# Kernel optimization log

Hardware: AMD Instinct MI355X
Metric: run time of the kernel (lower is better)

## Reference

```python
import jax, jax.numpy as jnp
import numpy as np

B, NUM, FEAT, H = 32, 512, 1024, 8
HLEN = FEAT // H  # 128


def setup_inputs() -> dict:
    key = jax.random.key(0)
    ks = jax.random.split(key, 9)
    x1 = jax.random.normal(ks[0], (B, NUM, FEAT), dtype=jnp.float32)
    x2 = jax.random.normal(ks[1], (B, NUM, FEAT), dtype=jnp.float32)
    adj = jax.random.uniform(ks[2], (B, NUM, NUM), dtype=jnp.float32)
    bias = jax.random.normal(ks[3], (B, NUM, NUM), dtype=jnp.float32)
    mask = jax.random.bernoulli(ks[4], 0.1, (B, 1, NUM, NUM))  # bool
    # per-head projection weights: FCNet([feat, hdim], '', 0.1) == Linear(feat, hdim)
    Wq = jax.random.normal(ks[5], (H, FEAT, HLEN), dtype=jnp.float32) * (1.0 / np.sqrt(FEAT))
    bq = jnp.zeros((H, HLEN), dtype=jnp.float32)
    # output FCNet([feat, feat], 'ReLU', 0.1) == Linear(feat, feat) + ReLU
    Wl = jax.random.normal(ks[6], (FEAT, FEAT), dtype=jnp.float32) * (1.0 / np.sqrt(FEAT))
    bl = jnp.zeros((FEAT,), dtype=jnp.float32)
    return {"x1": x1, "x2": x2, "adj": adj, "bias": bias, "mask": mask,
            "Wq": Wq, "bq": bq, "Wl": Wl, "bl": bl}


def reference(x1, x2, adj, bias, mask, Wq, bq, Wl, bl):
    # adj and bias are unused in the original forward.
    Bsz, num, feat = x1.shape
    h_len = feat // H
    # Q: concat of per-head Linear(feat, h_len) projections -> [B, num, feat],
    # then split into H heads of h_len: [B, H, num, h_len]
    Q = jnp.einsum('bnf,hfd->bhnd', x1, Wq) + bq[None, :, None, :]
    # K = V = x1 reshaped into heads
    K = x1.reshape(Bsz, num, H, h_len).transpose(0, 2, 1, 3)  # [B,H,num,h_len]
    V = K
    # gate: average pool x2 over its sequence dim -> [B, feat] -> [B,H,1,h_len]
    gate = jnp.mean(x2, axis=1).reshape(Bsz, 1, H, h_len).transpose(0, 2, 1, 3)
    scale = 1.0 / np.sqrt(float(h_len))
    aff = jnp.einsum('bhnd,bhmd->bhnm', Q * gate, K * gate) * scale
    L = jnp.where(mask, jnp.float32(-1e9), aff)
    att = jax.nn.softmax(L, axis=3)  # [B,H,num,num]
    V_ = jnp.einsum('bhnm,bhmd->bhnd', att, V)
    V_ = V_.transpose(0, 2, 1, 3).reshape(Bsz, num, feat)
    xout = jax.nn.relu(V_ @ Wl + bl) + x1
    return (xout, att)
```

## Files before the change

kernel.cpp:

```cpp
#include <hip/hip_runtime.h>
#include <hip/hip_bf16.h>

typedef __attribute__((ext_vector_type(8))) short s8v;
typedef __attribute__((ext_vector_type(4))) float f4v;
typedef __hip_bfloat16 bf16;

__device__ __forceinline__ unsigned short f2b(float f) {
  bf16 h = __float2bfloat16(f);
  return *reinterpret_cast<unsigned short*>(&h);
}

__global__ __launch_bounds__(256) void gate_kernel(const float* __restrict__ x2,
                                                   float* __restrict__ g2s) {
  __shared__ float red[256];
  const int b = blockIdx.x >> 4, fc = blockIdx.x & 15;
  const int fi = threadIdx.x & 63, ng = threadIdx.x >> 6;
  const int f = fc * 64 + fi;
  const float* p = x2 + (size_t)b * 524288 + f;
  float s = 0.f;
  for (int n = ng * 128; n < ng * 128 + 128; ++n) s += p[(size_t)n * 1024];
  red[threadIdx.x] = s;
  __syncthreads();
  if (threadIdx.x < 64) {
    float tot = red[fi] + red[fi + 64] + red[fi + 128] + red[fi + 192];
    float mean = tot * (1.0f / 512.0f);
    g2s[b * 1024 + f] = mean * mean * 0.08838834764831845f;
  }
}

__global__ __launch_bounds__(256) void cvt_f32_bf16(const float* __restrict__ in,
                                                    bf16* __restrict__ out, int n4) {
  int i = blockIdx.x * 256 + threadIdx.x;
  if (i >= n4) return;
  f4v v = reinterpret_cast<const f4v*>(in)[i];
  ushort4 o;
  o.x = f2b(v.x); o.y = f2b(v.y); o.z = f2b(v.z); o.w = f2b(v.w);
  reinterpret_cast<ushort4*>(out)[i] = o;
}

__global__ __launch_bounds__(256) void transpose_f32_bf16(
    const float* __restrict__ in, bf16* __restrict__ out,
    int in_rstride, int out_rstride, int hi_shift,
    long hi_mul, long lo_mul, long out_mul) {
  __shared__ float tile[32][33];
  const int z = blockIdx.z;
  const long in_off = (long)(z >> hi_shift) * hi_mul + (long)(z & ((1 << hi_shift) - 1)) * lo_mul;
  const int r0 = blockIdx.x * 32, c0 = blockIdx.y * 32;
  const int i = threadIdx.x >> 5, j = threadIdx.x & 31;
  const float* ip = in + in_off + (long)r0 * in_rstride + c0;
#pragma unroll
  for (int s = 0; s < 4; ++s) tile[i + s * 8][j] = ip[(long)(i + s * 8) * in_rstride + j];
  __syncthreads();
  bf16* op = out + (long)z * out_mul + (long)c0 * out_rstride + r0;
#pragma unroll
  for (int s = 0; s < 4; ++s) op[(long)(i + s * 8) * out_rstride + j] = __float2bfloat16(tile[j][i + s * 8]);
}

template <int EPI>
__global__ __launch_bounds__(256) void gemm_nt(
    const void* __restrict__ Ap, const bf16* __restrict__ BTp, void* __restrict__ Op,
    const float* __restrict__ e1, const float* __restrict__ e2,
    int K, int lda, int ldb) {
  constexpr bool AF32 = (EPI == 1);
  __shared__ alignas(16) bf16 As[128 * 40];
  __shared__ alignas(16) bf16 Bs[128 * 40];
  const int t = threadIdx.x;
  const int lane = t & 63;
  const int w = t >> 6;
  const int wr = w >> 1, wc = w & 1;
  const int lr = lane & 15, g = lane >> 4;
  const int z = blockIdx.z;
  const int m0 = blockIdx.x * 128, n0 = blockIdx.y * 128;

  const bf16* Ab = nullptr;
  const float* Af = nullptr;
  const bf16* BT = BTp;
  if constexpr (AF32) {
    Af = reinterpret_cast<const float*>(Ap) + (size_t)z * (512 * 512);
    BT = BTp + (size_t)z * (128 * 512);
  } else {
    Ab = reinterpret_cast<const bf16*>(Ap);
  }

  f4v acc[4][4];
#pragma unroll
  for (int i = 0; i < 4; ++i)
#pragma unroll
    for (int j = 0; j < 4; ++j) acc[i][j] = (f4v){0.f, 0.f, 0.f, 0.f};

  for (int k0 = 0; k0 < K; k0 += 32) {
    __syncthreads();
    if constexpr (AF32) {
#pragma unroll
      for (int i = 0; i < 4; ++i) {
        int c = t + i * 256;
        int r = c >> 3, q = c & 7;
        f4v v = *reinterpret_cast<const f4v*>(Af + (size_t)(m0 + r) * lda + k0 + q * 4);
        ushort4 o;
        o.x = f2b(v.x); o.y = f2b(v.y); o.z = f2b(v.z); o.w = f2b(v.w);
        *reinterpret_cast<ushort4*>(&As[r * 40 + q * 4]) = o;
      }
    } else {
#pragma unroll
      for (int i = 0; i < 2; ++i) {
        int c = t + i * 256;
        int r = c >> 2, q = c & 3;
        s8v v = *reinterpret_cast<const s8v*>(Ab + (size_t)(m0 + r) * lda + k0 + q * 8);
        *reinterpret_cast<s8v*>(&As[r * 40 + q * 8]) = v;
      }
    }
#pragma unroll
    for (int i = 0; i < 2; ++i) {
      int c = t + i * 256;
      int r = c >> 2, q = c & 3;
      s8v v = *reinterpret_cast<const s8v*>(BT + (size_t)(n0 + r) * ldb + k0 + q * 8);
      *reinterpret_cast<s8v*>(&Bs[r * 40 + q * 8]) = v;
    }
    __syncthreads();
    s8v af[4], bfr[4];
#pragma unroll
    for (int mi = 0; mi < 4; ++mi)
      af[mi] = *reinterpret_cast<const s8v*>(&As[(wr * 64 + mi * 16 + lr) * 40 + g * 8]);
#pragma unroll
    for (int ni = 0; ni < 4; ++ni)
      bfr[ni] = *reinterpret_cast<const s8v*>(&Bs[(wc * 64 + ni * 16 + lr) * 40 + g * 8]);
#pragma unroll
    for (int mi = 0; mi < 4; ++mi)
#pragma unroll
      for (int ni = 0; ni < 4; ++ni)
        acc[mi][ni] = __builtin_amdgcn_mfma_f32_16x16x32_bf16(af[mi], bfr[ni], acc[mi][ni], 0, 0, 0);
  }

#pragma unroll
  for (int mi = 0; mi < 4; ++mi) {
#pragma unroll
    for (int ni = 0; ni < 4; ++ni) {
#pragma unroll
      for (int v = 0; v < 4; ++v) {
        int row = m0 + wr * 64 + mi * 16 + g * 4 + v;
        int col = n0 + wc * 64 + ni * 16 + lr;
        float val = acc[mi][ni][v];
        if constexpr (EPI == 0) {
          float q = (val + e1[col]) * e2[(row >> 9) * 1024 + col];
          reinterpret_cast<bf16*>(Op)[(size_t)row * 1024 + col] = __float2bfloat16(q);
        } else if constexpr (EPI == 1) {
          int b = z >> 3, h = z & 7;
          reinterpret_cast<bf16*>(Op)[((size_t)(b * 512 + row)) * 1024 + h * 128 + col] =
              __float2bfloat16(val);
        } else {
          float r2 = fmaxf(val + e1[col], 0.f) + e2[(size_t)row * 1024 + col];
          reinterpret_cast<float*>(Op)[(size_t)row * 1024 + col] = r2;
        }
      }
    }
  }
}

__global__ __launch_bounds__(64) void attn_softmax(
    const bf16* __restrict__ Qs, const bf16* __restrict__ x1b,
    const int* __restrict__ mask, float* __restrict__ att) {
  const int bid = blockIdx.x;
  const int rt = bid & 31;
  const int bh = bid >> 5;
  const int h = bh & 7, b = bh >> 3;
  const int lane = threadIdx.x;
  const int lr = lane & 15, g = lane >> 4;
  const int n0 = rt * 16;

  const bf16* qrow = Qs + (size_t)(b * 512 + n0 + lr) * 1024 + h * 128;
  s8v a[4];
#pragma unroll
  for (int kt = 0; kt < 4; ++kt) a[kt] = *reinterpret_cast<const s8v*>(qrow + kt * 32 + g * 8);

  f4v acc[32];
#pragma unroll
  for (int mt = 0; mt < 32; ++mt) acc[mt] = (f4v){0.f, 0.f, 0.f, 0.f};

  const bf16* kbase = x1b + (size_t)b * 512 * 1024 + h * 128;
#pragma unroll
  for (int mt = 0; mt < 32; ++mt) {
    const bf16* krow = kbase + (size_t)(mt * 16 + lr) * 1024;
#pragma unroll
    for (int kt = 0; kt < 4; ++kt) {
      s8v bb = *reinterpret_cast<const s8v*>(krow + kt * 32 + g * 8);
      acc[mt] = __builtin_amdgcn_mfma_f32_16x16x32_bf16(a[kt], bb, acc[mt], 0, 0, 0);
    }
  }

  const int* mrow = mask + (size_t)b * 512 * 512 + (size_t)n0 * 512;
  float mx[4] = {-3e38f, -3e38f, -3e38f, -3e38f};
#pragma unroll
  for (int mt = 0; mt < 32; ++mt) {
#pragma unroll
    for (int v = 0; v < 4; ++v) {
      int row = g * 4 + v, col = mt * 16 + lr;
      float val = acc[mt][v];
      val = mrow[row * 512 + col] ? -1e9f : val;
      acc[mt][v] = val;
      mx[v] = fmaxf(mx[v], val);
    }
  }
#pragma unroll
  for (int v = 0; v < 4; ++v) {
    float m = mx[v];
    m = fmaxf(m, __shfl_xor(m, 1));
    m = fmaxf(m, __shfl_xor(m, 2));
    m = fmaxf(m, __shfl_xor(m, 4));
    m = fmaxf(m, __shfl_xor(m, 8));
    mx[v] = m;
  }
  float sm[4] = {0.f, 0.f, 0.f, 0.f};
#pragma unroll
  for (int mt = 0; mt < 32; ++mt) {
#pragma unroll
    for (int v = 0; v < 4; ++v) {
      float e = __expf(acc[mt][v] - mx[v]);
      acc[mt][v] = e;
      sm[v] += e;
    }
  }
#pragma unroll
  for (int v = 0; v < 4; ++v) {
    float s = sm[v];
    s += __shfl_xor(s, 1);
    s += __shfl_xor(s, 2);
    s += __shfl_xor(s, 4);
    s += __shfl_xor(s, 8);
    sm[v] = 1.0f / s;
  }
  float* orow = att + ((size_t)bh * 512 + n0) * 512;
#pragma unroll
  for (int mt = 0; mt < 32; ++mt) {
#pragma unroll
    for (int v = 0; v < 4; ++v) {
      orow[(g * 4 + v) * 512 + mt * 16 + lr] = acc[mt][v] * sm[v];
    }
  }
}

extern "C" void kernel_launch(void* const* d_in, const int* in_sizes, int n_in,
                              void* d_out, int out_size, void* d_ws, size_t ws_size,
                              hipStream_t stream) {
  (void)in_sizes; (void)n_in; (void)out_size; (void)ws_size;
  const float* x1 = (const float*)d_in[0];
  const float* x2 = (const float*)d_in[1];
  const int* mask = (const int*)d_in[4];
  const float* Wq = (const float*)d_in[5];
  const float* bq = (const float*)d_in[6];
  const float* Wl = (const float*)d_in[7];
  const float* bl = (const float*)d_in[8];

  float* xout = (float*)d_out;
  float* att = (float*)d_out + 16777216;

  char* ws = (char*)d_ws;
  bf16* x1b   = (bf16*)(ws);
  bf16* VT    = (bf16*)(ws + 33554432);
  bf16* Qs    = (bf16*)(ws + 67108864);
  bf16* WcatT = (bf16*)(ws + 100663296);
  bf16* WlT   = (bf16*)(ws + 102760448);
  float* g2s  = (float*)(ws + 104857600);

  gate_kernel<<<dim3(32 * 16), dim3(256), 0, stream>>>(x2, g2s);
  cvt_f32_bf16<<<dim3(16384), dim3(256), 0, stream>>>(x1, x1b, 4194304);
  transpose_f32_bf16<<<dim3(16, 4, 256), dim3(256), 0, stream>>>(
      x1, VT, 1024, 512, 3, (long)524288, (long)128, (long)65536);
  transpose_f32_bf16<<<dim3(32, 4, 8), dim3(256), 0, stream>>>(
      Wq, WcatT, 128, 1024, 0, (long)131072, (long)0, (long)131072);
  transpose_f32_bf16<<<dim3(32, 32, 1), dim3(256), 0, stream>>>(
      Wl, WlT, 1024, 1024, 0, (long)0, (long)0, (long)0);
  gemm_nt<0><<<dim3(128, 8, 1), dim3(256), 0, stream>>>(
      (const void*)x1b, WcatT, (void*)Qs, bq, g2s, 1024, 1024, 1024);
  attn_softmax<<<dim3(8192), dim3(64), 0, stream>>>(Qs, x1b, mask, att);
  gemm_nt<1><<<dim3(4, 1, 256), dim3(256), 0, stream>>>(
      (const void*)att, VT, (void*)x1b, nullptr, nullptr, 512, 512, 512);
  gemm_nt<2><<<dim3(128, 8, 1), dim3(256), 0, stream>>>(
      (const void*)x1b, WlT, (void*)xout, bl, x1, 1024, 1024, 1024);
}
```

Before: 917.1 us.

## Fuse attention-times-V into softmax kernel and use direct-to-LDS loads in GEMM

The attention-times-V product now runs inside the softmax kernel. Each wave writes its normalized bf16 probabilities to swizzled shared memory and multiplies them against the transposed V directly. This removes the separate batched GEMM, which had to re-read and convert the large fp32 attention matrix. The projection GEMMs now use global_load_lds 16-byte loads into an XOR-swizzled, unpadded LDS layout, with block-index remapping meant to improve L2 reuse. The fused output is written in place into the Q buffer, which relies on each wave reading its Q rows before overwriting them; the fused kernel also uses more LDS per block.

```diff
diff --git a/kernel.cpp b/kernel.cpp
--- a/kernel.cpp
+++ b/kernel.cpp
@@ -8,6 +8,12 @@
 __device__ __forceinline__ unsigned short f2b(float f) {
   bf16 h = __float2bfloat16(f);
   return *reinterpret_cast<unsigned short*>(&h);
+}
+
+__device__ __forceinline__ void gload16(const void* g, void* l) {
+  __builtin_amdgcn_global_load_lds(
+      (const __attribute__((address_space(1))) void*)g,
+      (__attribute__((address_space(3))) void*)l, 16, 0, 0);
 }
 
 __global__ __launch_bounds__(256) void gate_kernel(const float* __restrict__ x2,
@@ -58,29 +64,28 @@
 
 template <int EPI>
 __global__ __launch_bounds__(256) void gemm_nt(
-    const void* __restrict__ Ap, const bf16* __restrict__ BTp, void* __restrict__ Op,
-    const float* __restrict__ e1, const float* __restrict__ e2,
-    int K, int lda, int ldb) {
-  constexpr bool AF32 = (EPI == 1);
-  __shared__ alignas(16) bf16 As[128 * 40];
-  __shared__ alignas(16) bf16 Bs[128 * 40];
+    const bf16* __restrict__ A, const bf16* __restrict__ BT, void* __restrict__ Op,
+    const float* __restrict__ e1, const float* __restrict__ e2) {
+  __shared__ alignas(16) bf16 As[128 * 32];
+  __shared__ alignas(16) bf16 Bs[128 * 32];
   const int t = threadIdx.x;
   const int lane = t & 63;
-  const int w = t >> 6;
-  const int wr = w >> 1, wc = w & 1;
+  const int wv = t >> 6;
+  const int wr = wv >> 1, wc = wv & 1;
   const int lr = lane & 15, g = lane >> 4;
-  const int z = blockIdx.z;
-  const int m0 = blockIdx.x * 128, n0 = blockIdx.y * 128;
-
-  const bf16* Ab = nullptr;
-  const float* Af = nullptr;
-  const bf16* BT = BTp;
-  if constexpr (AF32) {
-    Af = reinterpret_cast<const float*>(Ap) + (size_t)z * (512 * 512);
-    BT = BTp + (size_t)z * (128 * 512);
-  } else {
-    Ab = reinterpret_cast<const bf16*>(Ap);
-  }
+  const int o = blockIdx.x;
+  const int wk = (o & 7) * 128 + (o >> 3);
+  const int m0 = (wk >> 3) * 128, n0 = (wk & 7) * 128;
+
+  const int cr = lane >> 2;
+  const int q = (lane & 3) ^ ((lane >> 3) & 3);
+  const int c0 = 2 * wv, c1 = 2 * wv + 1;
+  const bf16* gA0 = A + (size_t)(m0 + c0 * 16 + cr) * 1024 + q * 8;
+  const bf16* gA1 = A + (size_t)(m0 + c1 * 16 + cr) * 1024 + q * 8;
+  const bf16* gB0 = BT + (size_t)(n0 + c0 * 16 + cr) * 1024 + q * 8;
+  const bf16* gB1 = BT + (size_t)(n0 + c1 * 16 + cr) * 1024 + q * 8;
+  bf16* lA0 = &As[c0 * 512]; bf16* lA1 = &As[c1 * 512];
+  bf16* lB0 = &Bs[c0 * 512]; bf16* lB1 = &Bs[c1 * 512];
 
   f4v acc[4][4];
 #pragma unroll
@@ -88,42 +93,22 @@
 #pragma unroll
     for (int j = 0; j < 4; ++j) acc[i][j] = (f4v){0.f, 0.f, 0.f, 0.f};
 
-  for (int k0 = 0; k0 < K; k0 += 32) {
+  const int xr = (lr >> 1) & 3;
+
+  for (int k0 = 0; k0 < 1024; k0 += 32) {
     __syncthreads();
-    if constexpr (AF32) {
-#pragma unroll
-      for (int i = 0; i < 4; ++i) {
-        int c = t + i * 256;
-        int r = c >> 3, q = c & 7;
-        f4v v = *reinterpret_cast<const f4v*>(Af + (size_t)(m0 + r) * lda + k0 + q * 4);
-        ushort4 o;
-        o.x = f2b(v.x); o.y = f2b(v.y); o.z = f2b(v.z); o.w = f2b(v.w);
-        *reinterpret_cast<ushort4*>(&As[r * 40 + q * 4]) = o;
-      }
-    } else {
-#pragma unroll
-      for (int i = 0; i < 2; ++i) {
-        int c = t + i * 256;
-        int r = c >> 2, q = c & 3;
-        s8v v = *reinterpret_cast<const s8v*>(Ab + (size_t)(m0 + r) * lda + k0 + q * 8);
-        *reinterpret_cast<s8v*>(&As[r * 40 + q * 8]) = v;
-      }
-    }
-#pragma unroll
-    for (int i = 0; i < 2; ++i) {
-      int c = t + i * 256;
-      int r = c >> 2, q = c & 3;
-      s8v v = *reinterpret_cast<const s8v*>(BT + (size_t)(n0 + r) * ldb + k0 + q * 8);
-      *reinterpret_cast<s8v*>(&Bs[r * 40 + q * 8]) = v;
-    }
+    gload16(gA0 + k0, lA0);
+    gload16(gA1 + k0, lA1);
+    gload16(gB0 + k0, lB0);
+    gload16(gB1 + k0, lB1);
     __syncthreads();
     s8v af[4], bfr[4];
 #pragma unroll
     for (int mi = 0; mi < 4; ++mi)
-      af[mi] = *reinterpret_cast<const s8v*>(&As[(wr * 64 + mi * 16 + lr) * 40 + g * 8]);
+      af[mi] = *reinterpret_cast<const s8v*>(&As[(wr * 64 + mi * 16 + lr) * 32 + ((g ^ xr) * 8)]);
 #pragma unroll
     for (int ni = 0; ni < 4; ++ni)
-      bfr[ni] = *reinterpret_cast<const s8v*>(&Bs[(wc * 64 + ni * 16 + lr) * 40 + g * 8]);
+      bfr[ni] = *reinterpret_cast<const s8v*>(&Bs[(wc * 64 + ni * 16 + lr) * 32 + ((g ^ xr) * 8)]);
 #pragma unroll
     for (int mi = 0; mi < 4; ++mi)
 #pragma unroll
@@ -141,12 +126,8 @@
         int col = n0 + wc * 64 + ni * 16 + lr;
         float val = acc[mi][ni][v];
         if constexpr (EPI == 0) {
-          float q = (val + e1[col]) * e2[(row >> 9) * 1024 + col];
-          reinterpret_cast<bf16*>(Op)[(size_t)row * 1024 + col] = __float2bfloat16(q);
-        } else if constexpr (EPI == 1) {
-          int b = z >> 3, h = z & 7;
-          reinterpret_cast<bf16*>(Op)[((size_t)(b * 512 + row)) * 1024 + h * 128 + col] =
-              __float2bfloat16(val);
+          float qv = (val + e1[col]) * e2[(row >> 9) * 1024 + col];
+          reinterpret_cast<bf16*>(Op)[(size_t)row * 1024 + col] = __float2bfloat16(qv);
         } else {
           float r2 = fmaxf(val + e1[col], 0.f) + e2[(size_t)row * 1024 + col];
           reinterpret_cast<float*>(Op)[(size_t)row * 1024 + col] = r2;
@@ -156,16 +137,21 @@
   }
 }
 
-__global__ __launch_bounds__(64) void attn_softmax(
+__device__ __forceinline__ int fsw(int r) { return ((r >> 2) | ((r & 1) << 2)); }
+
+__global__ __launch_bounds__(256) void attn_fused(
     const bf16* __restrict__ Qs, const bf16* __restrict__ x1b,
-    const int* __restrict__ mask, float* __restrict__ att) {
-  const int bid = blockIdx.x;
-  const int rt = bid & 31;
-  const int bh = bid >> 5;
+    const bf16* __restrict__ VT, const int* __restrict__ mask,
+    float* __restrict__ att, bf16* __restrict__ Vout) {
+  __shared__ bf16 P[4][16 * 512];
+  const int o = blockIdx.x;
+  const int wk = (o & 7) * 256 + (o >> 3);
+  const int rt = wk & 7, bh = wk >> 3;
   const int h = bh & 7, b = bh >> 3;
-  const int lane = threadIdx.x;
+  const int wv = threadIdx.x >> 6;
+  const int lane = threadIdx.x & 63;
   const int lr = lane & 15, g = lane >> 4;
-  const int n0 = rt * 16;
+  const int n0 = rt * 64 + wv * 16;
 
   const bf16* qrow = Qs + (size_t)(b * 512 + n0 + lr) * 1024 + h * 128;
   s8v a[4];
@@ -176,7 +162,7 @@
 #pragma unroll
   for (int mt = 0; mt < 32; ++mt) acc[mt] = (f4v){0.f, 0.f, 0.f, 0.f};
 
-  const bf16* kbase = x1b + (size_t)b * 512 * 1024 + h * 128;
+  const bf16* kbase = x1b + (size_t)b * 524288 + h * 128;
 #pragma unroll
   for (int mt = 0; mt < 32; ++mt) {
     const bf16* krow = kbase + (size_t)(mt * 16 + lr) * 1024;
@@ -187,7 +173,7 @@
     }
   }
 
-  const int* mrow = mask + (size_t)b * 512 * 512 + (size_t)n0 * 512;
+  const int* mrow = mask + (size_t)b * 262144 + (size_t)n0 * 512;
   float mx[4] = {-3e38f, -3e38f, -3e38f, -3e38f};
 #pragma unroll
   for (int mt = 0; mt < 32; ++mt) {
@@ -228,12 +214,39 @@
     s += __shfl_xor(s, 8);
     sm[v] = 1.0f / s;
   }
+
   float* orow = att + ((size_t)bh * 512 + n0) * 512;
-#pragma unroll
-  for (int mt = 0; mt < 32; ++mt) {
-#pragma unroll
-    for (int v = 0; v < 4; ++v) {
-      orow[(g * 4 + v) * 512 + mt * 16 + lr] = acc[mt][v] * sm[v];
+  bf16* Pw = P[wv];
+#pragma unroll
+  for (int mt = 0; mt < 32; ++mt) {
+#pragma unroll
+    for (int v = 0; v < 4; ++v) {
+      int r = g * 4 + v, c = mt * 16 + lr;
+      float tv = acc[mt][v] * sm[v];
+      orow[r * 512 + c] = tv;
+      Pw[r * 512 + (c ^ (fsw(r) * 8))] = __float2bfloat16(tv);
+    }
+  }
+
+  s8v a2[16];
+  const int fx = fsw(lr) * 8;
+#pragma unroll
+  for (int kt = 0; kt < 16; ++kt)
+    a2[kt] = *reinterpret_cast<const s8v*>(&Pw[lr * 512 + ((kt * 32 + g * 8) ^ fx)]);
+
+  const bf16* vbase = VT + (size_t)bh * 65536;
+#pragma unroll
+  for (int nt = 0; nt < 8; ++nt) {
+    f4v oacc = (f4v){0.f, 0.f, 0.f, 0.f};
+#pragma unroll
+    for (int kt = 0; kt < 16; ++kt) {
+      s8v bb = *reinterpret_cast<const s8v*>(vbase + (size_t)(nt * 16 + lr) * 512 + kt * 32 + g * 8);
+      oacc = __builtin_amdgcn_mfma_f32_16x16x32_bf16(a2[kt], bb, oacc, 0, 0, 0);
+    }
+#pragma unroll
+    for (int v = 0; v < 4; ++v) {
+      Vout[(size_t)(b * 512 + n0 + g * 4 + v) * 1024 + h * 128 + nt * 16 + lr] =
+          __float2bfloat16(oacc[v]);
     }
   }
 }
@@ -269,11 +282,7 @@
       Wq, WcatT, 128, 1024, 0, (long)131072, (long)0, (long)131072);
   transpose_f32_bf16<<<dim3(32, 32, 1), dim3(256), 0, stream>>>(
       Wl, WlT, 1024, 1024, 0, (long)0, (long)0, (long)0);
-  gemm_nt<0><<<dim3(128, 8, 1), dim3(256), 0, stream>>>(
-      (const void*)x1b, WcatT, (void*)Qs, bq, g2s, 1024, 1024, 1024);
-  attn_softmax<<<dim3(8192), dim3(64), 0, stream>>>(Qs, x1b, mask, att);
-  gemm_nt<1><<<dim3(4, 1, 256), dim3(256), 0, stream>>>(
-      (const void*)att, VT, (void*)x1b, nullptr, nullptr, 512, 512, 512);
-  gemm_nt<2><<<dim3(128, 8, 1), dim3(256), 0, stream>>>(
-      (const void*)x1b, WlT, (void*)xout, bl, x1, 1024, 1024, 1024);
-}
+  gemm_nt<0><<<dim3(1024), dim3(256), 0, stream>>>(x1b, WcatT, (void*)Qs, bq, g2s);
+  attn_fused<<<dim3(2048), dim3(256), 0, stream>>>(Qs, x1b, VT, mask, att, Qs);
+  gemm_nt<2><<<dim3(1024), dim3(256), 0, stream>>>(Qs, WlT, (void*)xout, bl, x1);
+}
```

After: 901.8 us. Within noise of the previous version (-1.7%).
